# Kernel tuning notes

Measured on AMD Instinct MI355X. Metric: run time of the kernel, lower is better.

Reference implementation:

```python
import jax, jax.numpy as jnp
import numpy as np

B, S, H = 2, 2048, 2048
FFN = 1024
E = 8
TOP_K = 2


def setup_inputs() -> dict:
    key = jax.random.key(0)
    ks = jax.random.split(key, 5)
    scale = 0.02
    hidden_states = jax.random.normal(ks[0], (B, S, H), dtype=jnp.float32)
    Wg = jax.random.normal(ks[1], (E, H), dtype=jnp.float32) * scale   # gate: Linear(H, E) weight
    W1 = jax.random.normal(ks[2], (E, FFN, H), dtype=jnp.float32) * scale  # stacked w1 per expert
    W3 = jax.random.normal(ks[3], (E, FFN, H), dtype=jnp.float32) * scale  # stacked w3 per expert
    W2 = jax.random.normal(ks[4], (E, H, FFN), dtype=jnp.float32) * scale  # stacked w2 per expert
    bias = jnp.zeros((E,), dtype=jnp.float32)  # e_score_correction_bias buffer
    return {"hidden_states": hidden_states, "Wg": Wg, "W1": W1, "W2": W2, "W3": W3, "bias": bias}


def reference(hidden_states, Wg, W1, W2, W3, bias):
    bsz, seq_len, hidden_dim = hidden_states.shape
    x = hidden_states.reshape(-1, hidden_dim)                 # [T, H]
    router_logits = x @ Wg.T                                  # [T, E]
    routing_weights = jax.nn.sigmoid(router_logits.astype(jnp.float32))
    scores = routing_weights + bias                           # bias only affects selection
    _, top_k_index = jax.lax.top_k(scores, TOP_K)             # [T, K]
    top_k_weights = jnp.take_along_axis(routing_weights, top_k_index, axis=1)
    top_k_weights = top_k_weights / top_k_weights.sum(axis=-1, keepdims=True)
    top_k_weights = top_k_weights.astype(x.dtype)
    # per-token per-expert combine weight (0 for non-selected experts)
    one_hot = jax.nn.one_hot(top_k_index, Wg.shape[0], dtype=x.dtype)  # [T, K, E]
    expert_w = jnp.einsum('tk,tke->te', top_k_weights, one_hot)        # [T, E]
    # SwiGLU expert MLPs applied via stacked (grouped) GEMMs
    h1 = jnp.einsum('th,efh->tef', x, W1)                     # [T, E, FFN]
    h3 = jnp.einsum('th,efh->tef', x, W3)
    g = jax.nn.silu(h1) * h3 * expert_w[:, :, None]           # scale before down-proj
    out = jnp.einsum('tef,ehf->th', g, W2)                    # weighted combine
    return out.reshape(bsz, seq_len, hidden_dim)
```

## Files before the change

### kernel.cpp

```cpp
#include <hip/hip_runtime.h>
#include <hip/hip_bf16.h>


#define T_TOK 4096
#define H_DIM 2048
#define FFN_D 1024
#define NE    8

typedef __attribute__((ext_vector_type(8))) short          bf16x8;
typedef __attribute__((ext_vector_type(4))) float          f32x4;
typedef __attribute__((ext_vector_type(4))) unsigned short us4;
typedef __attribute__((ext_vector_type(8))) unsigned short us8;

#define RB_ROUTER 1024u

__device__ __forceinline__ unsigned short f2bf(float f) {
  unsigned u = __builtin_bit_cast(unsigned, f);
  u += 0x7fffu + ((u >> 16) & 1u);
  return (unsigned short)(u >> 16);
}
__device__ __forceinline__ float bf2f(unsigned short u) {
  return __builtin_bit_cast(float, ((unsigned)u) << 16);
}
__device__ __forceinline__ us8 f8bf(float4 a, float4 b) {
  union { us8 o; unsigned u[4]; } r;
  asm("v_cvt_pk_bf16_f32 %0, %1, %2" : "=v"(r.u[0]) : "v"(a.x), "v"(a.y));
  asm("v_cvt_pk_bf16_f32 %0, %1, %2" : "=v"(r.u[1]) : "v"(a.z), "v"(a.w));
  asm("v_cvt_pk_bf16_f32 %0, %1, %2" : "=v"(r.u[2]) : "v"(b.x), "v"(b.y));
  asm("v_cvt_pk_bf16_f32 %0, %1, %2" : "=v"(r.u[3]) : "v"(b.z), "v"(b.w));
  return r.o;
}
__device__ __forceinline__ void async16(const void* g, void* l) {
  __builtin_amdgcn_global_load_lds((const __attribute__((address_space(1))) void*)g,
                                   (__attribute__((address_space(3))) void*)l, 16, 0, 0);
}

__global__ void router_kernel(const float* __restrict__ x,
                              const float* __restrict__ Wg,
                              const float* __restrict__ bias,
                              unsigned* __restrict__ epair,
                              float* __restrict__ wpair,
                              unsigned short* __restrict__ Xb) {
  const int wv   = threadIdx.x >> 6;
  const int lane = threadIdx.x & 63;
  const int t    = blockIdx.x * 4 + wv;

  const float4* xr = (const float4*)(x + (size_t)t * H_DIM);
  us4*          xb = (us4*)(Xb + (size_t)t * H_DIM);

  float acc[NE];
#pragma unroll
  for (int e = 0; e < NE; e++) acc[e] = 0.f;

#pragma unroll
  for (int j = 0; j < 8; j++) {
    int i4 = j * 64 + lane;
    float4 v = xr[i4];
    us4 d; d.x = f2bf(v.x); d.y = f2bf(v.y); d.z = f2bf(v.z); d.w = f2bf(v.w);
    xb[i4] = d;
#pragma unroll
    for (int e = 0; e < NE; e++) {
      float4 w = ((const float4*)(Wg + e * H_DIM))[i4];
      acc[e] += v.x * w.x + v.y * w.y + v.z * w.z + v.w * w.w;
    }
  }
#pragma unroll
  for (int e = 0; e < NE; e++) {
#pragma unroll
    for (int m = 32; m >= 1; m >>= 1) acc[e] += __shfl_xor(acc[e], m, 64);
  }

  if (lane == 0) {
    float sig[NE], sc[NE];
#pragma unroll
    for (int e = 0; e < NE; e++) {
      sig[e] = 1.f / (1.f + expf(-acc[e]));
      sc[e]  = sig[e] + bias[e];
    }
    int i1 = 0; float v1 = sc[0];
#pragma unroll
    for (int e = 1; e < NE; e++) if (sc[e] > v1) { v1 = sc[e]; i1 = e; }
    int i2 = -1; float v2 = -1e30f;
#pragma unroll
    for (int e = 0; e < NE; e++) if (e != i1 && sc[e] > v2) { v2 = sc[e]; i2 = e; }
    float w1 = sig[i1], w2 = sig[i2];
    float s = w1 + w2;
    epair[t] = (unsigned)i1 | ((unsigned)i2 << 8);
    wpair[2 * t]     = w1 / s;
    wpair[2 * t + 1] = w2 / s;
  }
}

__global__ void compact_kernel(const unsigned* __restrict__ epair,
                               const float* __restrict__ wpair,
                               int* __restrict__ cnt,
                               int* __restrict__ base,
                               int* __restrict__ rows,
                               float* __restrict__ wts,
                               int* __restrict__ t2s) {
  const int e    = threadIdx.x >> 6;
  const int lane = threadIdx.x & 63;
  const unsigned long long ltmask = ((unsigned long long)1 << lane) - 1;
  __shared__ int cnts[NE];

  int count = 0;
  for (int c = 0; c < T_TOK; c += 64) {
    int t = c + lane;
    unsigned ep = epair[t];
    bool m1 = ((ep & 255u) == (unsigned)e);
    bool m2 = (((ep >> 8) & 255u) == (unsigned)e);
    unsigned long long b1 = __ballot(m1);
    if (m1) {
      int p = count + __popcll(b1 & ltmask);
      rows[e * T_TOK + p] = t;
      wts [e * T_TOK + p] = wpair[2 * t];
      t2s[2 * t] = (e << 12) | p;
    }
    count += __popcll(b1);
    unsigned long long b2 = __ballot(m2);
    if (m2) {
      int p = count + __popcll(b2 & ltmask);
      rows[e * T_TOK + p] = t;
      wts [e * T_TOK + p] = wpair[2 * t + 1];
      t2s[2 * t + 1] = (e << 12) | p;
    }
    count += __popcll(b2);
  }
  if (lane == 0) { cnts[e] = count; cnt[e] = count; }
  __syncthreads();
  if (threadIdx.x == 0) {
    int s = 0;
    for (int i = 0; i < NE; i++) { base[i] = s; s += cnts[i]; }
    base[NE] = s;
  }
}

__launch_bounds__(256)
__global__ void upproj_fast(const unsigned short* __restrict__ Xb,
                            const float* __restrict__ W1,
                            const float* __restrict__ W3,
                            const int* __restrict__ cnt,
                            const int* __restrict__ base,
                            const int* __restrict__ rows,
                            const float* __restrict__ wts,
                            unsigned short* __restrict__ G) {
  const int e  = blockIdx.z;
  const int m0 = blockIdx.y * 128;
  const int n0 = blockIdx.x * 64;
  const int ce = cnt[e];
  if (m0 >= ce) return;

  __shared__ __align__(16) unsigned short As [128 * 32];
  __shared__ __align__(16) unsigned short B1s[64 * 32];
  __shared__ __align__(16) unsigned short B3s[64 * 32];
  __shared__ int   t_ids[128];
  __shared__ float w_lds[128];

  const int tid = threadIdx.x;
  if (tid < 128) {
    int i = m0 + tid;
    if (i < ce) { t_ids[tid] = rows[e * T_TOK + i]; w_lds[tid] = wts[e * T_TOK + i]; }
    else        { t_ids[tid] = 0;                   w_lds[tid] = 0.f; }
  }
  __syncthreads();

  const int lane = tid & 63;
  const int wv   = tid >> 6;

  const unsigned short* gA[2];
#pragma unroll
  for (int c = 0; c < 2; c++) {
    int r = wv * 32 + c * 16 + (lane >> 2);
    gA[c] = Xb + (size_t)t_ids[r] * H_DIM + (lane & 3) * 8;
  }
  unsigned short* lA0 = &As[(wv * 32 + 0)  * 32];
  unsigned short* lA1 = &As[(wv * 32 + 16) * 32];

  const int brow = n0 + wv * 16 + (lane >> 2);
  const float* gB1 = W1 + (size_t)e * FFN_D * H_DIM + (size_t)brow * H_DIM + (lane & 3) * 8;
  const float* gB3 = W3 + (size_t)e * FFN_D * H_DIM + (size_t)brow * H_DIM + (lane & 3) * 8;
  const int bidx = (wv * 16 + (lane >> 2)) * 32 + (lane & 3) * 8;

  const int wm = (wv & 1) * 64;
  const int wn = (wv >> 1) * 32;
  const int qk = (lane >> 4) * 8;
  const int lr = lane & 15;

  f32x4 acc1[4][2], acc3[4][2];
#pragma unroll
  for (int mi = 0; mi < 4; mi++)
#pragma unroll
    for (int ni = 0; ni < 2; ni++) { acc1[mi][ni] = (f32x4)0.f; acc3[mi][ni] = (f32x4)0.f; }

  float4 p0 = *(const float4*)(gB1 + 0);
  float4 p1 = *(const float4*)(gB1 + 4);
  float4 p2 = *(const float4*)(gB3 + 0);
  float4 p3 = *(const float4*)(gB3 + 4);

  for (int kt = 0; kt < H_DIM; kt += 32) {
    async16(gA[0] + kt, lA0);
    async16(gA[1] + kt, lA1);
    *(us8*)&B1s[bidx] = f8bf(p0, p1);
    *(us8*)&B3s[bidx] = f8bf(p2, p3);
    __syncthreads();

    if (kt + 32 < H_DIM) {
      p0 = *(const float4*)(gB1 + kt + 32);
      p1 = *(const float4*)(gB1 + kt + 36);
      p2 = *(const float4*)(gB3 + kt + 32);
      p3 = *(const float4*)(gB3 + kt + 36);
    }

    bf16x8 a[4], b1[2], b3[2];
#pragma unroll
    for (int mi = 0; mi < 4; mi++)
      a[mi] = *(const bf16x8*)&As[(wm + mi * 16 + lr) * 32 + qk];
#pragma unroll
    for (int ni = 0; ni < 2; ni++) {
      b1[ni] = *(const bf16x8*)&B1s[(wn + ni * 16 + lr) * 32 + qk];
      b3[ni] = *(const bf16x8*)&B3s[(wn + ni * 16 + lr) * 32 + qk];
    }
#pragma unroll
    for (int mi = 0; mi < 4; mi++)
#pragma unroll
      for (int ni = 0; ni < 2; ni++) {
        acc1[mi][ni] = __builtin_amdgcn_mfma_f32_16x16x32_bf16(a[mi], b1[ni], acc1[mi][ni], 0, 0, 0);
        acc3[mi][ni] = __builtin_amdgcn_mfma_f32_16x16x32_bf16(a[mi], b3[ni], acc3[mi][ni], 0, 0, 0);
      }
    __syncthreads();
  }

  const int be = base[e];
#pragma unroll
  for (int mi = 0; mi < 4; mi++)
#pragma unroll
    for (int ni = 0; ni < 2; ni++)
#pragma unroll
      for (int r = 0; r < 4; r++) {
        int row = wm + mi * 16 + (lane >> 4) * 4 + r;
        int col = wn + ni * 16 + lr;
        int i = m0 + row;
        if (i < ce) {
          float h1 = acc1[mi][ni][r];
          float h3 = acc3[mi][ni][r];
          float g  = h1 / (1.f + expf(-h1)) * h3 * w_lds[row];
          G[(size_t)(be + i) * FFN_D + n0 + col] = f2bf(g);
        }
      }
}

__launch_bounds__(256)
__global__ void downproj_fast(const unsigned short* __restrict__ G,
                              const float* __restrict__ W2,
                              const int* __restrict__ cnt,
                              const int* __restrict__ base,
                              unsigned short* __restrict__ Gd) {
  const int e  = blockIdx.z;
  const int m0 = blockIdx.y * 128;
  const int n0 = blockIdx.x * 128;
  const int ce = cnt[e];
  if (m0 >= ce) return;
  const int be = base[e];

  __shared__ __align__(16) unsigned short As[128 * 32];
  __shared__ __align__(16) unsigned short Bs[128 * 32];

  const int tid  = threadIdx.x;
  const int lane = tid & 63;
  const int wv   = tid >> 6;

  const unsigned short* gA[2];
#pragma unroll
  for (int c = 0; c < 2; c++) {
    int r = m0 + wv * 32 + c * 16 + (lane >> 2);
    if (r >= ce) r = ce - 1;
    gA[c] = G + (size_t)(be + r) * FFN_D + (lane & 3) * 8;
  }
  unsigned short* lA[2] = { &As[(wv * 32 + 0) * 32], &As[(wv * 32 + 16) * 32] };

  const int rb0 = wv * 32 + (lane >> 2);
  const int rb1 = rb0 + 16;
  const float* gB0 = W2 + (size_t)e * H_DIM * FFN_D + (size_t)(n0 + rb0) * FFN_D + (lane & 3) * 8;
  const float* gB1 = W2 + (size_t)e * H_DIM * FFN_D + (size_t)(n0 + rb1) * FFN_D + (lane & 3) * 8;
  const int bi0 = rb0 * 32 + (lane & 3) * 8;
  const int bi1 = rb1 * 32 + (lane & 3) * 8;

  const int wm = (wv & 1) * 64;
  const int wn = (wv >> 1) * 64;
  const int qk = (lane >> 4) * 8;
  const int lr = lane & 15;

  f32x4 acc[4][4];
#pragma unroll
  for (int mi = 0; mi < 4; mi++)
#pragma unroll
    for (int ni = 0; ni < 4; ni++) acc[mi][ni] = (f32x4)0.f;

  float4 p0 = *(const float4*)(gB0 + 0);
  float4 p1 = *(const float4*)(gB0 + 4);
  float4 p2 = *(const float4*)(gB1 + 0);
  float4 p3 = *(const float4*)(gB1 + 4);

  for (int kt = 0; kt < FFN_D; kt += 32) {
    async16(gA[0] + kt, lA[0]);
    async16(gA[1] + kt, lA[1]);
    *(us8*)&Bs[bi0] = f8bf(p0, p1);
    *(us8*)&Bs[bi1] = f8bf(p2, p3);
    __syncthreads();

    if (kt + 32 < FFN_D) {
      p0 = *(const float4*)(gB0 + kt + 32);
      p1 = *(const float4*)(gB0 + kt + 36);
      p2 = *(const float4*)(gB1 + kt + 32);
      p3 = *(const float4*)(gB1 + kt + 36);
    }

    bf16x8 a[4], b[4];
#pragma unroll
    for (int mi = 0; mi < 4; mi++)
      a[mi] = *(const bf16x8*)&As[(wm + mi * 16 + lr) * 32 + qk];
#pragma unroll
    for (int ni = 0; ni < 4; ni++)
      b[ni] = *(const bf16x8*)&Bs[(wn + ni * 16 + lr) * 32 + qk];
#pragma unroll
    for (int mi = 0; mi < 4; mi++)
#pragma unroll
      for (int ni = 0; ni < 4; ni++)
        acc[mi][ni] = __builtin_amdgcn_mfma_f32_16x16x32_bf16(a[mi], b[ni], acc[mi][ni], 0, 0, 0);
    __syncthreads();
  }

#pragma unroll
  for (int mi = 0; mi < 4; mi++)
#pragma unroll
    for (int ni = 0; ni < 4; ni++)
#pragma unroll
      for (int r = 0; r < 4; r++) {
        int row = wm + mi * 16 + (lane >> 4) * 4 + r;
        int col = wn + ni * 16 + lr;
        int i = m0 + row;
        if (i < ce)
          Gd[(size_t)(be + i) * H_DIM + n0 + col] = f2bf(acc[mi][ni][r]);
      }
}

__global__ void combine_kernel(const unsigned short* __restrict__ Gd,
                               const int* __restrict__ base,
                               const int* __restrict__ tok2slot,
                               float* __restrict__ out) {
  const int t = blockIdx.x;
  const int v1 = tok2slot[2 * t], v2 = tok2slot[2 * t + 1];
  const int s1 = base[v1 >> 12] + (v1 & 4095);
  const int s2 = base[v2 >> 12] + (v2 & 4095);
  const us4* r1 = (const us4*)(Gd + (size_t)s1 * H_DIM);
  const us4* r2 = (const us4*)(Gd + (size_t)s2 * H_DIM);
  float4* o = (float4*)(out + (size_t)t * H_DIM);
#pragma unroll
  for (int j = 0; j < 2; j++) {
    int i = j * 256 + threadIdx.x;
    us4 a = r1[i], b = r2[i];
    float4 r;
    r.x = bf2f(a.x) + bf2f(b.x);
    r.y = bf2f(a.y) + bf2f(b.y);
    r.z = bf2f(a.z) + bf2f(b.z);
    r.w = bf2f(a.w) + bf2f(b.w);
    o[i] = r;
  }
}

extern "C" void kernel_launch(void* const* d_in, const int* in_sizes, int n_in,
                              void* d_out, int out_size, void* d_ws, size_t ws_size,
                              hipStream_t stream) {
  (void)in_sizes; (void)n_in; (void)out_size; (void)ws_size;
  const float* x    = (const float*)d_in[0];
  const float* Wg   = (const float*)d_in[1];
  const float* W1   = (const float*)d_in[2];
  const float* W2   = (const float*)d_in[3];
  const float* W3   = (const float*)d_in[4];
  const float* bias = (const float*)d_in[5];
  float* out = (float*)d_out;

  char* ws = (char*)d_ws;
  const size_t OFF_CNT   = 0;
  const size_t OFF_BASE  = 64;
  const size_t OFF_T2S   = 1024;
  const size_t OFF_ROWS  = 65536;
  const size_t OFF_WTS   = OFF_ROWS + 131072;
  const size_t OFF_EPAIR = OFF_WTS + 131072;
  const size_t OFF_WPAIR = OFF_EPAIR + 16384;
  const size_t OFF_XB    = 1048576;
  const size_t OFF_G     = OFF_XB + 16777216;
  const size_t OFF_GD    = OFF_G + 16777216;

  int*   cnt   = (int*)(ws + OFF_CNT);
  int*   base  = (int*)(ws + OFF_BASE);
  int*   t2s   = (int*)(ws + OFF_T2S);
  int*   rows  = (int*)(ws + OFF_ROWS);
  float* wts   = (float*)(ws + OFF_WTS);
  unsigned* epair = (unsigned*)(ws + OFF_EPAIR);
  float* wpair = (float*)(ws + OFF_WPAIR);
  unsigned short* Xb  = (unsigned short*)(ws + OFF_XB);
  unsigned short* G   = (unsigned short*)(ws + OFF_G);
  unsigned short* Gd  = (unsigned short*)(ws + OFF_GD);

  router_kernel<<<RB_ROUTER, 256, 0, stream>>>(x, Wg, bias, epair, wpair, Xb);

  compact_kernel<<<1, 512, 0, stream>>>(epair, wpair, cnt, base, rows, wts, t2s);

  dim3 g2(FFN_D / 64, T_TOK / 128, NE);
  upproj_fast<<<g2, 256, 0, stream>>>(Xb, W1, W3, cnt, base, rows, wts, G);

  dim3 g3(H_DIM / 128, T_TOK / 128, NE);
  downproj_fast<<<g3, 256, 0, stream>>>(G, W2, cnt, base, Gd);

  combine_kernel<<<T_TOK, 256, 0, stream>>>(Gd, base, t2s, out);
}
```

Measured before the change: 467.5 us.

## Double-buffer LDS tiles and XOR-swizzle layout in expert up/down projection GEMMs

```diff
diff --git a/kernel.cpp b/kernel.cpp
--- a/kernel.cpp
+++ b/kernel.cpp
@@ -150,9 +150,9 @@
   const int ce = cnt[e];
   if (m0 >= ce) return;
 
-  __shared__ __align__(16) unsigned short As [128 * 32];
-  __shared__ __align__(16) unsigned short B1s[64 * 32];
-  __shared__ __align__(16) unsigned short B3s[64 * 32];
+  __shared__ __align__(16) unsigned short As [2][128 * 32];
+  __shared__ __align__(16) unsigned short B1s[2][64 * 32];
+  __shared__ __align__(16) unsigned short B3s[2][64 * 32];
   __shared__ int   t_ids[128];
   __shared__ float w_lds[128];
 
@@ -167,23 +167,25 @@
   const int lane = tid & 63;
   const int wv   = tid >> 6;
 
+  const int sA   = (lane >> 3) & 3;
+  const int gcol = ((lane & 3) ^ sA) * 8;
+  const int rxor = ((lane & 15) >> 1) & 3;
+  const int qx   = (((lane >> 4) ^ rxor)) * 8;
+
   const unsigned short* gA[2];
 #pragma unroll
   for (int c = 0; c < 2; c++) {
     int r = wv * 32 + c * 16 + (lane >> 2);
-    gA[c] = Xb + (size_t)t_ids[r] * H_DIM + (lane & 3) * 8;
-  }
-  unsigned short* lA0 = &As[(wv * 32 + 0)  * 32];
-  unsigned short* lA1 = &As[(wv * 32 + 16) * 32];
+    gA[c] = Xb + (size_t)t_ids[r] * H_DIM + gcol;
+  }
 
   const int brow = n0 + wv * 16 + (lane >> 2);
   const float* gB1 = W1 + (size_t)e * FFN_D * H_DIM + (size_t)brow * H_DIM + (lane & 3) * 8;
   const float* gB3 = W3 + (size_t)e * FFN_D * H_DIM + (size_t)brow * H_DIM + (lane & 3) * 8;
-  const int bidx = (wv * 16 + (lane >> 2)) * 32 + (lane & 3) * 8;
+  const int bidx = (wv * 16 + (lane >> 2)) * 32 + (((lane & 3) ^ sA)) * 8;
 
   const int wm = (wv & 1) * 64;
   const int wn = (wv >> 1) * 32;
-  const int qk = (lane >> 4) * 8;
   const int lr = lane & 15;
 
   f32x4 acc1[4][2], acc3[4][2];
@@ -192,33 +194,38 @@
 #pragma unroll
     for (int ni = 0; ni < 2; ni++) { acc1[mi][ni] = (f32x4)0.f; acc3[mi][ni] = (f32x4)0.f; }
 
+  async16(gA[0], &As[0][(wv * 32 + 0)  * 32 ]);
+  async16(gA[1], &As[0][(wv * 32 + 16) * 32 ]);
   float4 p0 = *(const float4*)(gB1 + 0);
   float4 p1 = *(const float4*)(gB1 + 4);
   float4 p2 = *(const float4*)(gB3 + 0);
   float4 p3 = *(const float4*)(gB3 + 4);
-
+  asm volatile("s_waitcnt vmcnt(0)" ::: "memory");
+  *(us8*)&B1s[0][bidx] = f8bf(p0, p1);
+  *(us8*)&B3s[0][bidx] = f8bf(p2, p3);
+  __syncthreads();
+
+  int cur = 0;
   for (int kt = 0; kt < H_DIM; kt += 32) {
-    async16(gA[0] + kt, lA0);
-    async16(gA[1] + kt, lA1);
-    *(us8*)&B1s[bidx] = f8bf(p0, p1);
-    *(us8*)&B3s[bidx] = f8bf(p2, p3);
-    __syncthreads();
-
-    if (kt + 32 < H_DIM) {
+    const int notlast = (kt + 32 < H_DIM);
+    if (notlast) {
+      async16(gA[0] + kt + 32, &As[cur ^ 1][(wv * 32 + 0)  * 32 ]);
+      async16(gA[1] + kt + 32, &As[cur ^ 1][(wv * 32 + 16) * 32 ]);
       p0 = *(const float4*)(gB1 + kt + 32);
       p1 = *(const float4*)(gB1 + kt + 36);
       p2 = *(const float4*)(gB3 + kt + 32);
       p3 = *(const float4*)(gB3 + kt + 36);
     }
+    __builtin_amdgcn_sched_barrier(0);
 
     bf16x8 a[4], b1[2], b3[2];
 #pragma unroll
     for (int mi = 0; mi < 4; mi++)
-      a[mi] = *(const bf16x8*)&As[(wm + mi * 16 + lr) * 32 + qk];
+      a[mi] = *(const bf16x8*)&As[cur][(wm + mi * 16 + lr) * 32 + qx];
 #pragma unroll
     for (int ni = 0; ni < 2; ni++) {
-      b1[ni] = *(const bf16x8*)&B1s[(wn + ni * 16 + lr) * 32 + qk];
-      b3[ni] = *(const bf16x8*)&B3s[(wn + ni * 16 + lr) * 32 + qk];
+      b1[ni] = *(const bf16x8*)&B1s[cur][(wn + ni * 16 + lr) * 32 + qx];
+      b3[ni] = *(const bf16x8*)&B3s[cur][(wn + ni * 16 + lr) * 32 + qx];
     }
 #pragma unroll
     for (int mi = 0; mi < 4; mi++)
@@ -227,7 +234,17 @@
         acc1[mi][ni] = __builtin_amdgcn_mfma_f32_16x16x32_bf16(a[mi], b1[ni], acc1[mi][ni], 0, 0, 0);
         acc3[mi][ni] = __builtin_amdgcn_mfma_f32_16x16x32_bf16(a[mi], b3[ni], acc3[mi][ni], 0, 0, 0);
       }
-    __syncthreads();
+
+    if (notlast) {
+      asm volatile("s_waitcnt vmcnt(0)" ::: "memory");
+      *(us8*)&B1s[cur ^ 1][bidx] = f8bf(p0, p1);
+      *(us8*)&B3s[cur ^ 1][bidx] = f8bf(p2, p3);
+      asm volatile("s_waitcnt lgkmcnt(0)" ::: "memory");
+      __builtin_amdgcn_sched_barrier(0);
+      __builtin_amdgcn_s_barrier();
+      __builtin_amdgcn_sched_barrier(0);
+    }
+    cur ^= 1;
   }
 
   const int be = base[e];
@@ -262,32 +279,36 @@
   if (m0 >= ce) return;
   const int be = base[e];
 
-  __shared__ __align__(16) unsigned short As[128 * 32];
-  __shared__ __align__(16) unsigned short Bs[128 * 32];
+  __shared__ __align__(16) unsigned short As[2][128 * 32];
+  __shared__ __align__(16) unsigned short Bs[2][128 * 32];
 
   const int tid  = threadIdx.x;
   const int lane = tid & 63;
   const int wv   = tid >> 6;
 
+  const int sA   = (lane >> 3) & 3;
+  const int gcol = ((lane & 3) ^ sA) * 8;
+  const int rxor = ((lane & 15) >> 1) & 3;
+  const int qx   = (((lane >> 4) ^ rxor)) * 8;
+
   const unsigned short* gA[2];
 #pragma unroll
   for (int c = 0; c < 2; c++) {
     int r = m0 + wv * 32 + c * 16 + (lane >> 2);
     if (r >= ce) r = ce - 1;
-    gA[c] = G + (size_t)(be + r) * FFN_D + (lane & 3) * 8;
-  }
-  unsigned short* lA[2] = { &As[(wv * 32 + 0) * 32], &As[(wv * 32 + 16) * 32] };
+    gA[c] = G + (size_t)(be + r) * FFN_D + gcol;
+  }
 
   const int rb0 = wv * 32 + (lane >> 2);
   const int rb1 = rb0 + 16;
   const float* gB0 = W2 + (size_t)e * H_DIM * FFN_D + (size_t)(n0 + rb0) * FFN_D + (lane & 3) * 8;
   const float* gB1 = W2 + (size_t)e * H_DIM * FFN_D + (size_t)(n0 + rb1) * FFN_D + (lane & 3) * 8;
-  const int bi0 = rb0 * 32 + (lane & 3) * 8;
-  const int bi1 = rb1 * 32 + (lane & 3) * 8;
+  const int bw  = ((lane & 3) ^ sA) * 8;
+  const int bi0 = rb0 * 32 + bw;
+  const int bi1 = rb1 * 32 + bw;
 
   const int wm = (wv & 1) * 64;
   const int wn = (wv >> 1) * 64;
-  const int qk = (lane >> 4) * 8;
   const int lr = lane & 15;
 
   f32x4 acc[4][4];
@@ -296,38 +317,53 @@
 #pragma unroll
     for (int ni = 0; ni < 4; ni++) acc[mi][ni] = (f32x4)0.f;
 
+  async16(gA[0], &As[0][(wv * 32 + 0)  * 32 ]);
+  async16(gA[1], &As[0][(wv * 32 + 16) * 32 ]);
   float4 p0 = *(const float4*)(gB0 + 0);
   float4 p1 = *(const float4*)(gB0 + 4);
   float4 p2 = *(const float4*)(gB1 + 0);
   float4 p3 = *(const float4*)(gB1 + 4);
-
+  asm volatile("s_waitcnt vmcnt(0)" ::: "memory");
+  *(us8*)&Bs[0][bi0] = f8bf(p0, p1);
+  *(us8*)&Bs[0][bi1] = f8bf(p2, p3);
+  __syncthreads();
+
+  int cur = 0;
   for (int kt = 0; kt < FFN_D; kt += 32) {
-    async16(gA[0] + kt, lA[0]);
-    async16(gA[1] + kt, lA[1]);
-    *(us8*)&Bs[bi0] = f8bf(p0, p1);
-    *(us8*)&Bs[bi1] = f8bf(p2, p3);
-    __syncthreads();
-
-    if (kt + 32 < FFN_D) {
+    const int notlast = (kt + 32 < FFN_D);
+    if (notlast) {
+      async16(gA[0] + kt + 32, &As[cur ^ 1][(wv * 32 + 0)  * 32 ]);
+      async16(gA[1] + kt + 32, &As[cur ^ 1][(wv * 32 + 16) * 32 ]);
       p0 = *(const float4*)(gB0 + kt + 32);
       p1 = *(const float4*)(gB0 + kt + 36);
       p2 = *(const float4*)(gB1 + kt + 32);
       p3 = *(const float4*)(gB1 + kt + 36);
     }
+    __builtin_amdgcn_sched_barrier(0);
 
     bf16x8 a[4], b[4];
 #pragma unroll
     for (int mi = 0; mi < 4; mi++)
-      a[mi] = *(const bf16x8*)&As[(wm + mi * 16 + lr) * 32 + qk];
+      a[mi] = *(const bf16x8*)&As[cur][(wm + mi * 16 + lr) * 32 + qx];
 #pragma unroll
     for (int ni = 0; ni < 4; ni++)
-      b[ni] = *(const bf16x8*)&Bs[(wn + ni * 16 + lr) * 32 + qk];
+      b[ni] = *(const bf16x8*)&Bs[cur][(wn + ni * 16 + lr) * 32 + qx];
 #pragma unroll
     for (int mi = 0; mi < 4; mi++)
 #pragma unroll
       for (int ni = 0; ni < 4; ni++)
         acc[mi][ni] = __builtin_amdgcn_mfma_f32_16x16x32_bf16(a[mi], b[ni], acc[mi][ni], 0, 0, 0);
-    __syncthreads();
+
+    if (notlast) {
+      asm volatile("s_waitcnt vmcnt(0)" ::: "memory");
+      *(us8*)&Bs[cur ^ 1][bi0] = f8bf(p0, p1);
+      *(us8*)&Bs[cur ^ 1][bi1] = f8bf(p2, p3);
+      asm volatile("s_waitcnt lgkmcnt(0)" ::: "memory");
+      __builtin_amdgcn_sched_barrier(0);
+      __builtin_amdgcn_s_barrier();
+      __builtin_amdgcn_sched_barrier(0);
+    }
+    cur ^= 1;
   }
 
 #pragma unroll
```

After: 492.0 us. +5.2%, slower.
